# Performance work log

Hardware: AMD Instinct MI355X
Metric: run time of the kernel (lower is better)

Reference implementation:

```python
import jax, jax.numpy as jnp
import numpy as np

T = 2048            # context_length
C = 1024            # embedding size
HEAD_QK = 256       # config.head_qk_size
VOCAB = 50257       # config.vocab_size


def setup_inputs() -> dict:
    key = jax.random.key(0)
    k1, k2, k3, k4 = jax.random.split(key, 4)
    x = jax.random.normal(k1, (T, C), dtype=jnp.float32)
    idx = jax.random.randint(k2, (T,), 0, VOCAB, dtype=jnp.int32)
    # Dense kernels (flax Dense stores kernel as [in, out], no bias)
    Wq = jax.random.normal(k3, (C, HEAD_QK), dtype=jnp.float32) / np.sqrt(C)
    Wk = jax.random.normal(k4, (C, HEAD_QK), dtype=jnp.float32) / np.sqrt(C)
    return {"x": x, "idx": idx, "Wq": Wq, "Wk": Wk}


def reference(x, idx, Wq, Wk):
    # q, k: [T, HEAD_QK]
    q = x @ Wq
    k = x @ Wk
    # causal-masked, softmax-free scores: [T, T]
    c = (q @ k.T) * (1.0 / HEAD_QK)
    causal = jnp.tril(jnp.ones((T, T), dtype=bool))
    c = jnp.where(causal, c, 0.0)
    # c @ one_hot(idx, VOCAB) == segment-sum of c's columns by token id
    # out[t, v] = sum_{s : idx[s] == v} c[t, s]   -> [T, VOCAB]
    out = jax.ops.segment_sum(c.T, idx, num_segments=VOCAB).T
    return out
```

## Files before the change

kernel.cpp:

```cpp
#include <hip/hip_runtime.h>

#define T_CTX 2048
#define C_DIM 1024
#define HQK   256
#define NVOC  50257

typedef float nfloat4 __attribute__((ext_vector_type(4)));
typedef _Float16 h2 __attribute__((ext_vector_type(2)));
typedef _Float16 h4 __attribute__((ext_vector_type(4)));

#if defined(__has_builtin)
#if __has_builtin(__builtin_amdgcn_fdot2)
#define HAVE_FDOT2 1
#endif
#endif
__device__ __forceinline__ float fdot2acc(h2 a, h2 b, float c) {
#ifdef HAVE_FDOT2
    return __builtin_amdgcn_fdot2(a, b, c, false);
#else
    return c + (float)a.x * (float)b.x + (float)a.y * (float)b.y;
#endif
}

__global__ __launch_bounds__(1024) void k_build_first(const int* __restrict__ idx,
                                                      int* __restrict__ first,
                                                      int* __restrict__ vocab_map) {
    __shared__ int sidx[T_CTX];
    __shared__ int skey[4096];
    __shared__ int sval[4096];
    const int tid = threadIdx.x;
    for (int i = tid; i < T_CTX; i += 1024) sidx[i] = idx[i];
    for (int i = tid; i < 4096; i += 1024) { skey[i] = -1; sval[i] = 0x7fffffff; }
    int4* vm4 = reinterpret_cast<int4*>(vocab_map);
    const int4 neg1 = make_int4(-1, -1, -1, -1);
    for (int i = tid; i < 12564; i += 1024) vm4[i] = neg1;
    if (tid == 0) vocab_map[NVOC - 1] = -1;
    __syncthreads();
#pragma unroll
    for (int rep = 0; rep < 2; ++rep) {
        const int s = tid + rep * 1024;
        const int my = sidx[s];
        int h = (int)(((unsigned)my * 2654435761u) >> 16) & 4095;
        while (true) {
            int k = skey[h];
            if (k == my) break;
            if (k == -1) {
                int old = atomicCAS(&skey[h], -1, my);
                if (old == -1 || old == my) break;
            }
            h = (h + 1) & 4095;
        }
        atomicMin(&sval[h], s);
    }
    __syncthreads();
#pragma unroll
    for (int rep = 0; rep < 2; ++rep) {
        const int s = tid + rep * 1024;
        const int my = sidx[s];
        int h = (int)(((unsigned)my * 2654435761u) >> 16) & 4095;
        while (skey[h] != my) h = (h + 1) & 4095;
        const int mp = sval[h];
        first[s] = mp;
        if (mp == s) vocab_map[my] = s;
    }
}

__global__ __launch_bounds__(512) void k_gemm_qk(const float* __restrict__ x,
                                                 const float* __restrict__ Wq,
                                                 const float* __restrict__ Wk,
                                                 _Float16* __restrict__ qbuf_h,
                                                 _Float16* __restrict__ kTh) {
    __shared__ h2 As2[16 * 68];
    __shared__ _Float16 BsH[16 * 136];
    const int row0 = blockIdx.x * 64;
    const int col0 = blockIdx.y * 64;
    const bool is_q = (col0 < HQK);
    const float* __restrict__ W = is_q ? Wq : Wk;
    const int wc0 = is_q ? col0 : (col0 - HQK);
    const int tid = threadIdx.x;
    const int tr = (tid >> 4) << 1;
    const int tc = (tid & 15) << 2;
    const int ar = tid >> 3, ak = (tid & 7) << 2;
    const int bk = tid >> 4, bc = (tid & 15) << 2;
    float acc[2][4] = {};
    for (int k0 = 0; k0 < C_DIM; k0 += 32) {
        float4 a4 = *reinterpret_cast<const float4*>(&x[(size_t)(row0 + ar) * C_DIM + k0 + ak]);
        float4 b4 = *reinterpret_cast<const float4*>(&W[(size_t)(k0 + bk) * HQK + wc0 + bc]);
        As2[(ak >> 1) * 68 + ar]       = h2{(_Float16)a4.x, (_Float16)a4.y};
        As2[((ak >> 1) + 1) * 68 + ar] = h2{(_Float16)a4.z, (_Float16)a4.w};
        {
            const int r = (bk >> 1) * 136, p = bk & 1;
            BsH[r + ((bc + 0) << 1) + p] = (_Float16)b4.x;
            BsH[r + ((bc + 1) << 1) + p] = (_Float16)b4.y;
            BsH[r + ((bc + 2) << 1) + p] = (_Float16)b4.z;
            BsH[r + ((bc + 3) << 1) + p] = (_Float16)b4.w;
        }
        __syncthreads();
#pragma unroll
        for (int kk2 = 0; kk2 < 16; ++kk2) {
            h2 a0 = As2[kk2 * 68 + tr];
            h2 a1 = As2[kk2 * 68 + tr + 1];
            const h2* bp = reinterpret_cast<const h2*>(&BsH[kk2 * 136 + (tc << 1)]);
            h2 b0 = bp[0], b1 = bp[1], b2 = bp[2], b3 = bp[3];
            acc[0][0] = fdot2acc(a0, b0, acc[0][0]); acc[0][1] = fdot2acc(a0, b1, acc[0][1]);
            acc[0][2] = fdot2acc(a0, b2, acc[0][2]); acc[0][3] = fdot2acc(a0, b3, acc[0][3]);
            acc[1][0] = fdot2acc(a1, b0, acc[1][0]); acc[1][1] = fdot2acc(a1, b1, acc[1][1]);
            acc[1][2] = fdot2acc(a1, b2, acc[1][2]); acc[1][3] = fdot2acc(a1, b3, acc[1][3]);
        }
        __syncthreads();
    }
    if (is_q) {
#pragma unroll
        for (int i = 0; i < 2; ++i) {
            h4 o = {(_Float16)acc[i][0], (_Float16)acc[i][1], (_Float16)acc[i][2], (_Float16)acc[i][3]};
            *reinterpret_cast<h4*>(&qbuf_h[(size_t)(row0 + tr + i) * HQK + col0 + tc]) = o;
        }
    } else {
#pragma unroll
        for (int j = 0; j < 4; ++j) {
            h2 o = {(_Float16)acc[0][j], (_Float16)acc[1][j]};
            *reinterpret_cast<h2*>(&kTh[(size_t)(wc0 + tc + j) * T_CTX + row0 + tr]) = o;
        }
    }
}

__global__ __launch_bounds__(512) void k_scores_gemm(const _Float16* __restrict__ q,
                                                     const _Float16* __restrict__ kTh,
                                                     float* __restrict__ c) {
    const int bt = blockIdx.x, bs = blockIdx.y;
    if (bs > bt) return;
    __shared__ h2 As2[16 * 68];
    __shared__ _Float16 BsH[16 * 136];
    const int row0 = bt * 64;
    const int col0 = bs * 64;
    const int tid = threadIdx.x;
    const int tr = (tid >> 4) << 1;
    const int tc = (tid & 15) << 2;
    const int ar = tid >> 3, ak = (tid & 7) << 2;
    const int bk = tid >> 4, bc = (tid & 15) << 2;
    float acc[2][4] = {};
    for (int k0 = 0; k0 < HQK; k0 += 32) {
        h4 a4 = *reinterpret_cast<const h4*>(&q[(size_t)(row0 + ar) * HQK + k0 + ak]);
        h4 b4 = *reinterpret_cast<const h4*>(&kTh[(size_t)(k0 + bk) * T_CTX + col0 + bc]);
        As2[(ak >> 1) * 68 + ar]       = h2{a4.x, a4.y};
        As2[((ak >> 1) + 1) * 68 + ar] = h2{a4.z, a4.w};
        {
            const int r = (bk >> 1) * 136, p = bk & 1;
            BsH[r + ((bc + 0) << 1) + p] = b4.x;
            BsH[r + ((bc + 1) << 1) + p] = b4.y;
            BsH[r + ((bc + 2) << 1) + p] = b4.z;
            BsH[r + ((bc + 3) << 1) + p] = b4.w;
        }
        __syncthreads();
#pragma unroll
        for (int kk2 = 0; kk2 < 16; ++kk2) {
            h2 a0 = As2[kk2 * 68 + tr];
            h2 a1 = As2[kk2 * 68 + tr + 1];
            const h2* bp = reinterpret_cast<const h2*>(&BsH[kk2 * 136 + (tc << 1)]);
            h2 b0 = bp[0], b1 = bp[1], b2 = bp[2], b3 = bp[3];
            acc[0][0] = fdot2acc(a0, b0, acc[0][0]); acc[0][1] = fdot2acc(a0, b1, acc[0][1]);
            acc[0][2] = fdot2acc(a0, b2, acc[0][2]); acc[0][3] = fdot2acc(a0, b3, acc[0][3]);
            acc[1][0] = fdot2acc(a1, b0, acc[1][0]); acc[1][1] = fdot2acc(a1, b1, acc[1][1]);
            acc[1][2] = fdot2acc(a1, b2, acc[1][2]); acc[1][3] = fdot2acc(a1, b3, acc[1][3]);
        }
        __syncthreads();
    }
    const float scale = 1.0f / 256.0f;
#pragma unroll
    for (int i = 0; i < 2; ++i) {
        float4 o = {acc[i][0] * scale, acc[i][1] * scale, acc[i][2] * scale, acc[i][3] * scale};
        *reinterpret_cast<float4*>(&c[(size_t)(row0 + tr + i) * T_CTX + col0 + tc]) = o;
    }
}

__global__ __launch_bounds__(256) void k_fold_expand(const float* __restrict__ c,
                                                     const int* __restrict__ first,
                                                     const int* __restrict__ vocab_map,
                                                     float* __restrict__ out) {
    __shared__ float rowc[T_CTX];
    const int t = blockIdx.x;
    for (int i = threadIdx.x; i < T_CTX; i += 256) rowc[i] = 0.0f;
    __syncthreads();
    const int nq = (t >> 2) + 1;
    for (int qd = threadIdx.x; qd < nq; qd += 256) {
        const int s0 = qd << 2;
        float4 v = *reinterpret_cast<const float4*>(&c[(size_t)t * T_CTX + s0]);
        int4 f4 = *reinterpret_cast<const int4*>(&first[s0]);
        if (s0 + 3 <= t) {
            atomicAdd(&rowc[f4.x], v.x); atomicAdd(&rowc[f4.y], v.y);
            atomicAdd(&rowc[f4.z], v.z); atomicAdd(&rowc[f4.w], v.w);
        } else {
            atomicAdd(&rowc[f4.x], v.x);
            if (s0 + 1 <= t) atomicAdd(&rowc[f4.y], v.y);
            if (s0 + 2 <= t) atomicAdd(&rowc[f4.z], v.z);
            if (s0 + 3 <= t) atomicAdd(&rowc[f4.w], v.w);
        }
    }
    __syncthreads();
    float* __restrict__ orow = out + (size_t)t * NVOC;
    const int lead = (4 - (t & 3)) & 3;
    if ((int)threadIdx.x < lead) {
        int m = vocab_map[threadIdx.x];
        orow[threadIdx.x] = (m >= 0) ? rowc[m] : 0.0f;
    }
    const int nvec = (NVOC - lead) >> 2;
    for (int i = threadIdx.x; i < nvec; i += 256) {
        const int v = lead + (i << 2);
        int m0 = vocab_map[v + 0], m1 = vocab_map[v + 1];
        int m2 = vocab_map[v + 2], m3 = vocab_map[v + 3];
        nfloat4 o;
        o.x = (m0 >= 0) ? rowc[m0] : 0.0f;
        o.y = (m1 >= 0) ? rowc[m1] : 0.0f;
        o.z = (m2 >= 0) ? rowc[m2] : 0.0f;
        o.w = (m3 >= 0) ? rowc[m3] : 0.0f;
        __builtin_nontemporal_store(o, reinterpret_cast<nfloat4*>(&orow[v]));
    }
    for (int v = lead + (nvec << 2) + threadIdx.x; v < NVOC; v += 256) {
        int m = vocab_map[v];
        orow[v] = (m >= 0) ? rowc[m] : 0.0f;
    }
}

extern "C" void kernel_launch(void* const* d_in, const int* in_sizes, int n_in,
                              void* d_out, int out_size, void* d_ws, size_t ws_size,
                              hipStream_t stream) {
    const float* x   = (const float*)d_in[0];
    const int*   idx = (const int*)d_in[1];
    const float* Wq  = (const float*)d_in[2];
    const float* Wk  = (const float*)d_in[3];
    float* out = (float*)d_out;

    char* ws = (char*)d_ws;
    _Float16* qbuf_h  = (_Float16*)(ws);
    _Float16* kTh     = (_Float16*)(ws + (1u << 20));
    float*    c       = (float*)(ws + (2u << 20));
    int*      first   = (int*)(ws + (18u << 20));
    int*      vocab_map = (int*)(ws + (18u << 20) + (16u << 10));

    k_build_first<<<1, 1024, 0, stream>>>(idx, first, vocab_map);
    dim3 gg(32, 8);
    k_gemm_qk<<<gg, 512, 0, stream>>>(x, Wq, Wk, qbuf_h, kTh);
    dim3 gs(32, 32);
    k_scores_gemm<<<gs, 512, 0, stream>>>(qbuf_h, kTh, c);
    k_fold_expand<<<T_CTX, 256, 0, stream>>>(c, first, vocab_map, out);
}
```

Before: 537.2 us.

## Use MFMA for score GEMM and skip vocab lookups via occupancy bitmap

The score GEMM now uses MFMA 16x16x32 f16 instructions, reading q and a row-major K directly from global memory with no LDS staging, so the K projection is stored untransposed. A bitmap of occupied vocab quads is also built in the first-occurrence kernel. The expand kernel uses it to write zero vectors for empty quads without gathering vocab_map, cutting gather reads from the large output pass. The risks are uncoalesced scalar stores in the MFMA epilogue and extra bitmap loads per block.

```diff
diff --git a/kernel.cpp b/kernel.cpp
--- a/kernel.cpp
+++ b/kernel.cpp
@@ -4,10 +4,13 @@
 #define C_DIM 1024
 #define HQK   256
 #define NVOC  50257
+#define NBMW  394
 
 typedef float nfloat4 __attribute__((ext_vector_type(4)));
 typedef _Float16 h2 __attribute__((ext_vector_type(2)));
 typedef _Float16 h4 __attribute__((ext_vector_type(4)));
+typedef _Float16 h8 __attribute__((ext_vector_type(8)));
+typedef float f32x4 __attribute__((ext_vector_type(4)));
 
 #if defined(__has_builtin)
 #if __has_builtin(__builtin_amdgcn_fdot2)
@@ -24,13 +27,16 @@
 
 __global__ __launch_bounds__(1024) void k_build_first(const int* __restrict__ idx,
                                                       int* __restrict__ first,
-                                                      int* __restrict__ vocab_map) {
+                                                      int* __restrict__ vocab_map,
+                                                      unsigned* __restrict__ bm) {
     __shared__ int sidx[T_CTX];
     __shared__ int skey[4096];
     __shared__ int sval[4096];
+    __shared__ unsigned sbm[NBMW];
     const int tid = threadIdx.x;
     for (int i = tid; i < T_CTX; i += 1024) sidx[i] = idx[i];
     for (int i = tid; i < 4096; i += 1024) { skey[i] = -1; sval[i] = 0x7fffffff; }
+    for (int i = tid; i < NBMW; i += 1024) sbm[i] = 0u;
     int4* vm4 = reinterpret_cast<int4*>(vocab_map);
     const int4 neg1 = make_int4(-1, -1, -1, -1);
     for (int i = tid; i < 12564; i += 1024) vm4[i] = neg1;
@@ -61,21 +67,28 @@
         while (skey[h] != my) h = (h + 1) & 4095;
         const int mp = sval[h];
         first[s] = mp;
-        if (mp == s) vocab_map[my] = s;
-    }
+        if (mp == s) {
+            vocab_map[my] = s;
+            const int qd = my >> 2;
+            atomicOr(&sbm[qd >> 5], 1u << (qd & 31));
+        }
+    }
+    __syncthreads();
+    for (int i = tid; i < NBMW; i += 1024) bm[i] = sbm[i];
 }
 
 __global__ __launch_bounds__(512) void k_gemm_qk(const float* __restrict__ x,
                                                  const float* __restrict__ Wq,
                                                  const float* __restrict__ Wk,
                                                  _Float16* __restrict__ qbuf_h,
-                                                 _Float16* __restrict__ kTh) {
+                                                 _Float16* __restrict__ kbuf_h) {
     __shared__ h2 As2[16 * 68];
     __shared__ _Float16 BsH[16 * 136];
     const int row0 = blockIdx.x * 64;
     const int col0 = blockIdx.y * 64;
     const bool is_q = (col0 < HQK);
     const float* __restrict__ W = is_q ? Wq : Wk;
+    _Float16* __restrict__ obuf = is_q ? qbuf_h : kbuf_h;
     const int wc0 = is_q ? col0 : (col0 - HQK);
     const int tid = threadIdx.x;
     const int tr = (tid >> 4) << 1;
@@ -109,77 +122,53 @@
         }
         __syncthreads();
     }
-    if (is_q) {
-#pragma unroll
-        for (int i = 0; i < 2; ++i) {
-            h4 o = {(_Float16)acc[i][0], (_Float16)acc[i][1], (_Float16)acc[i][2], (_Float16)acc[i][3]};
-            *reinterpret_cast<h4*>(&qbuf_h[(size_t)(row0 + tr + i) * HQK + col0 + tc]) = o;
-        }
-    } else {
-#pragma unroll
-        for (int j = 0; j < 4; ++j) {
-            h2 o = {(_Float16)acc[0][j], (_Float16)acc[1][j]};
-            *reinterpret_cast<h2*>(&kTh[(size_t)(wc0 + tc + j) * T_CTX + row0 + tr]) = o;
-        }
-    }
-}
-
-__global__ __launch_bounds__(512) void k_scores_gemm(const _Float16* __restrict__ q,
-                                                     const _Float16* __restrict__ kTh,
+#pragma unroll
+    for (int i = 0; i < 2; ++i) {
+        h4 o = {(_Float16)acc[i][0], (_Float16)acc[i][1], (_Float16)acc[i][2], (_Float16)acc[i][3]};
+        *reinterpret_cast<h4*>(&obuf[(size_t)(row0 + tr + i) * HQK + wc0 + tc]) = o;
+    }
+}
+
+__global__ __launch_bounds__(256) void k_scores_mfma(const _Float16* __restrict__ q,
+                                                     const _Float16* __restrict__ kb,
                                                      float* __restrict__ c) {
     const int bt = blockIdx.x, bs = blockIdx.y;
     if (bs > bt) return;
-    __shared__ h2 As2[16 * 68];
-    __shared__ _Float16 BsH[16 * 136];
-    const int row0 = bt * 64;
-    const int col0 = bs * 64;
-    const int tid = threadIdx.x;
-    const int tr = (tid >> 4) << 1;
-    const int tc = (tid & 15) << 2;
-    const int ar = tid >> 3, ak = (tid & 7) << 2;
-    const int bk = tid >> 4, bc = (tid & 15) << 2;
-    float acc[2][4] = {};
+    const int row0 = bt * 64, col0 = bs * 64;
+    const int w = threadIdx.x >> 6;
+    const int lane = threadIdx.x & 63;
+    const int arow = row0 + 16 * w + (lane & 15);
+    const int kgrp = (lane >> 4) << 3;
+    f32x4 acc[4] = {};
+#pragma unroll
     for (int k0 = 0; k0 < HQK; k0 += 32) {
-        h4 a4 = *reinterpret_cast<const h4*>(&q[(size_t)(row0 + ar) * HQK + k0 + ak]);
-        h4 b4 = *reinterpret_cast<const h4*>(&kTh[(size_t)(k0 + bk) * T_CTX + col0 + bc]);
-        As2[(ak >> 1) * 68 + ar]       = h2{a4.x, a4.y};
-        As2[((ak >> 1) + 1) * 68 + ar] = h2{a4.z, a4.w};
-        {
-            const int r = (bk >> 1) * 136, p = bk & 1;
-            BsH[r + ((bc + 0) << 1) + p] = b4.x;
-            BsH[r + ((bc + 1) << 1) + p] = b4.y;
-            BsH[r + ((bc + 2) << 1) + p] = b4.z;
-            BsH[r + ((bc + 3) << 1) + p] = b4.w;
-        }
-        __syncthreads();
-#pragma unroll
-        for (int kk2 = 0; kk2 < 16; ++kk2) {
-            h2 a0 = As2[kk2 * 68 + tr];
-            h2 a1 = As2[kk2 * 68 + tr + 1];
-            const h2* bp = reinterpret_cast<const h2*>(&BsH[kk2 * 136 + (tc << 1)]);
-            h2 b0 = bp[0], b1 = bp[1], b2 = bp[2], b3 = bp[3];
-            acc[0][0] = fdot2acc(a0, b0, acc[0][0]); acc[0][1] = fdot2acc(a0, b1, acc[0][1]);
-            acc[0][2] = fdot2acc(a0, b2, acc[0][2]); acc[0][3] = fdot2acc(a0, b3, acc[0][3]);
-            acc[1][0] = fdot2acc(a1, b0, acc[1][0]); acc[1][1] = fdot2acc(a1, b1, acc[1][1]);
-            acc[1][2] = fdot2acc(a1, b2, acc[1][2]); acc[1][3] = fdot2acc(a1, b3, acc[1][3]);
-        }
-        __syncthreads();
+        h8 a = *reinterpret_cast<const h8*>(&q[(size_t)arow * HQK + k0 + kgrp]);
+#pragma unroll
+        for (int ct = 0; ct < 4; ++ct) {
+            h8 b = *reinterpret_cast<const h8*>(&kb[(size_t)(col0 + 16 * ct + (lane & 15)) * HQK + k0 + kgrp]);
+            acc[ct] = __builtin_amdgcn_mfma_f32_16x16x32_f16(a, b, acc[ct], 0, 0, 0);
+        }
     }
     const float scale = 1.0f / 256.0f;
-#pragma unroll
-    for (int i = 0; i < 2; ++i) {
-        float4 o = {acc[i][0] * scale, acc[i][1] * scale, acc[i][2] * scale, acc[i][3] * scale};
-        *reinterpret_cast<float4*>(&c[(size_t)(row0 + tr + i) * T_CTX + col0 + tc]) = o;
-    }
+    const int orow = row0 + 16 * w + ((lane >> 4) << 2);
+    const int ocol = col0 + (lane & 15);
+#pragma unroll
+    for (int ct = 0; ct < 4; ++ct)
+#pragma unroll
+        for (int r = 0; r < 4; ++r)
+            c[(size_t)(orow + r) * T_CTX + ocol + 16 * ct] = acc[ct][r] * scale;
 }
 
 __global__ __launch_bounds__(256) void k_fold_expand(const float* __restrict__ c,
                                                      const int* __restrict__ first,
                                                      const int* __restrict__ vocab_map,
+                                                     const unsigned* __restrict__ bm,
                                                      float* __restrict__ out) {
     __shared__ float rowc[T_CTX];
+    __shared__ unsigned sbm[NBMW];
     const int t = blockIdx.x;
     for (int i = threadIdx.x; i < T_CTX; i += 256) rowc[i] = 0.0f;
+    for (int i = threadIdx.x; i < NBMW; i += 256) sbm[i] = bm[i];
     __syncthreads();
     const int nq = (t >> 2) + 1;
     for (int qd = threadIdx.x; qd < nq; qd += 256) {
@@ -204,16 +193,23 @@
         orow[threadIdx.x] = (m >= 0) ? rowc[m] : 0.0f;
     }
     const int nvec = (NVOC - lead) >> 2;
+    const nfloat4 z4 = {0.0f, 0.0f, 0.0f, 0.0f};
     for (int i = threadIdx.x; i < nvec; i += 256) {
         const int v = lead + (i << 2);
-        int m0 = vocab_map[v + 0], m1 = vocab_map[v + 1];
-        int m2 = vocab_map[v + 2], m3 = vocab_map[v + 3];
-        nfloat4 o;
-        o.x = (m0 >= 0) ? rowc[m0] : 0.0f;
-        o.y = (m1 >= 0) ? rowc[m1] : 0.0f;
-        o.z = (m2 >= 0) ? rowc[m2] : 0.0f;
-        o.w = (m3 >= 0) ? rowc[m3] : 0.0f;
-        __builtin_nontemporal_store(o, reinterpret_cast<nfloat4*>(&orow[v]));
+        const int q0 = v >> 2, q1 = (v + 3) >> 2;
+        const unsigned hit = ((sbm[q0 >> 5] >> (q0 & 31)) | (sbm[q1 >> 5] >> (q1 & 31))) & 1u;
+        if (hit) {
+            int m0 = vocab_map[v + 0], m1 = vocab_map[v + 1];
+            int m2 = vocab_map[v + 2], m3 = vocab_map[v + 3];
+            nfloat4 o;
+            o.x = (m0 >= 0) ? rowc[m0] : 0.0f;
+            o.y = (m1 >= 0) ? rowc[m1] : 0.0f;
+            o.z = (m2 >= 0) ? rowc[m2] : 0.0f;
+            o.w = (m3 >= 0) ? rowc[m3] : 0.0f;
+            __builtin_nontemporal_store(o, reinterpret_cast<nfloat4*>(&orow[v]));
+        } else {
+            __builtin_nontemporal_store(z4, reinterpret_cast<nfloat4*>(&orow[v]));
+        }
     }
     for (int v = lead + (nvec << 2) + threadIdx.x; v < NVOC; v += 256) {
         int m = vocab_map[v];
@@ -231,16 +227,17 @@
     float* out = (float*)d_out;
 
     char* ws = (char*)d_ws;
-    _Float16* qbuf_h  = (_Float16*)(ws);
-    _Float16* kTh     = (_Float16*)(ws + (1u << 20));
-    float*    c       = (float*)(ws + (2u << 20));
-    int*      first   = (int*)(ws + (18u << 20));
+    _Float16* qbuf_h   = (_Float16*)(ws);
+    _Float16* kbuf_h   = (_Float16*)(ws + (1u << 20));
+    float*    c        = (float*)(ws + (2u << 20));
+    int*      first    = (int*)(ws + (18u << 20));
     int*      vocab_map = (int*)(ws + (18u << 20) + (16u << 10));
-
-    k_build_first<<<1, 1024, 0, stream>>>(idx, first, vocab_map);
+    unsigned* bm       = (unsigned*)(ws + (19u << 20));
+
+    k_build_first<<<1, 1024, 0, stream>>>(idx, first, vocab_map, bm);
     dim3 gg(32, 8);
-    k_gemm_qk<<<gg, 512, 0, stream>>>(x, Wq, Wk, qbuf_h, kTh);
+    k_gemm_qk<<<gg, 512, 0, stream>>>(x, Wq, Wk, qbuf_h, kbuf_h);
     dim3 gs(32, 32);
-    k_scores_gemm<<<gs, 512, 0, stream>>>(qbuf_h, kTh, c);
-    k_fold_expand<<<T_CTX, 256, 0, stream>>>(c, first, vocab_map, out);
-}
+    k_scores_mfma<<<gs, 256, 0, stream>>>(qbuf_h, kbuf_h, c);
+    k_fold_expand<<<T_CTX, 256, 0, stream>>>(c, first, vocab_map, bm, out);
+}
```

Measured after the change: 536.6 us. About the same (-0.1%).
